# Performance work log

Hardware: AMD Instinct MI355X
Metric: run time of the kernel (lower is better)

## Reference

```python
import jax, jax.numpy as jnp
import numpy as np

B, N, T, D, H = 4, 8, 512, 256, 8
DK = D // H


def _dwconv(x, w, b=None):
    # x: (BN, D, T) depthwise conv, kernel 3, padding 'same', groups=D
    y = jax.lax.conv_general_dilated(
        x, w, window_strides=(1,), padding='SAME',
        feature_group_count=x.shape[1],
        dimension_numbers=('NCH', 'OIH', 'NCH'))
    if b is not None:
        y = y + b[None, :, None]
    return y


def setup_inputs() -> dict:
    key = jax.random.key(0)
    ks = jax.random.split(key, 16)
    s = 1.0 / np.sqrt(D)
    s3 = 1.0 / np.sqrt(3 * D)
    inp = {
        'query': jax.random.normal(ks[0], (B, N, T, D), jnp.float32),
        'key': jax.random.normal(ks[1], (B, N, T, D), jnp.float32),
        'value': jax.random.normal(ks[2], (B, N, T, D), jnp.float32),
        'key_padding_mask': jax.random.randint(ks[3], (B, N, T), 0, 2, jnp.int32),
        # depthwise conv params
        'w_pos': jax.random.uniform(ks[4], (D, 1, 3), jnp.float32, -0.577, 0.577),
        'b_pos': jax.random.uniform(ks[5], (D,), jnp.float32, -0.577, 0.577),
        # physics-initialized differential operators (still learnable floats)
        'w_vel': jnp.tile(jnp.array([-1.0, 0.0, 1.0], jnp.float32)[None, None, :], (D, 1, 1)),
        'w_acc': jnp.tile(jnp.array([1.0, -2.0, 1.0], jnp.float32)[None, None, :], (D, 1, 1)),
        # fusion / projection linears (stored as (in, out))
        'Wq': jax.random.uniform(ks[6], (3 * D, D), jnp.float32, -s3, s3),
        'bq': jax.random.uniform(ks[7], (D,), jnp.float32, -s3, s3),
        'Wk': jax.random.uniform(ks[8], (3 * D, D), jnp.float32, -s3, s3),
        'bk': jax.random.uniform(ks[9], (D,), jnp.float32, -s3, s3),
        'Wv': jax.random.uniform(ks[10], (D, D), jnp.float32, -s, s),
        'bv': jax.random.uniform(ks[11], (D,), jnp.float32, -s, s),
        'Wo': jax.random.uniform(ks[12], (D, D), jnp.float32, -s, s),
        'bo': jax.random.uniform(ks[13], (D,), jnp.float32, -s, s),
    }
    return inp


def reference(query, key, value, key_padding_mask,
              w_pos, b_pos, w_vel, w_acc,
              Wq, bq, Wk, bk, Wv, bv, Wo, bo):
    b, n, t, d = query.shape
    scale = jnp.float32(1.0 / np.sqrt(DK))

    def kin_feats(x):
        xin = x.reshape(b * n, t, d).transpose(0, 2, 1)  # (BN, D, T)
        p = _dwconv(xin, w_pos, b_pos)
        v = _dwconv(xin, w_vel)
        a = _dwconv(xin, w_acc)
        return jnp.concatenate([p, v, a], axis=1).transpose(0, 2, 1)  # (BN, T, 3D)

    qc = kin_feats(query)
    kc = kin_feats(key)

    Q = (qc @ Wq + bq).reshape(b, n, t, H, DK).transpose(0, 1, 3, 2, 4)  # (B,N,H,Tq,dk)
    K = (kc @ Wk + bk).reshape(b, n, t, H, DK).transpose(0, 1, 3, 2, 4)
    V = (value @ Wv + bv).reshape(b, n, t, H, DK).transpose(0, 1, 3, 2, 4)

    scores = jnp.einsum('bnhqd,bnhkd->bnhqk', Q, K) * scale
    mask = key_padding_mask.astype(bool)[:, :, None, None, :]  # (B,N,1,1,Tk)
    scores = jnp.where(mask, jnp.float32(-1e9), scores)
    attn = jax.nn.softmax(scores, axis=-1)  # dropout is identity in eval

    ctx = jnp.einsum('bnhqk,bnhkd->bnhqd', attn, V)
    ctx = ctx.transpose(0, 1, 3, 2, 4).reshape(b, n, t, d)
    return ctx @ Wo + bo
```

## Files before the change

kernel.cpp:

```cpp
#include <hip/hip_runtime.h>
#include <math.h>


typedef __attribute__((ext_vector_type(8))) short bf16x8;
typedef __attribute__((ext_vector_type(4))) float f32x4;
typedef __attribute__((ext_vector_type(16))) float f32x16;
typedef __attribute__((ext_vector_type(4))) int i32x4;

__device__ __forceinline__ unsigned short f2bf(float f) {
    unsigned u = __float_as_uint(f);
    return (unsigned short)((u + 0x7fff + ((u >> 16) & 1)) >> 16);
}
__device__ __forceinline__ float bf2f(unsigned short h) {
    return __uint_as_float(((unsigned)h) << 16);
}
__device__ __forceinline__ float ex2(float x) {
    float r; asm("v_exp_f32 %0, %1" : "=v"(r) : "v"(x)); return r;
}
__device__ __forceinline__ int cvtpk(float lo, float hi) {
    int r; asm("v_cvt_pk_bf16_f32 %0, %1, %2" : "=v"(r) : "v"(lo), "v"(hi)); return r;
}
__device__ __forceinline__ void gll16(const void* gsrc, const void* ldst) {
    __builtin_amdgcn_global_load_lds(
        (const __attribute__((address_space(1))) unsigned int*)gsrc,
        (__attribute__((address_space(3))) unsigned int*)ldst, 16, 0, 0);
}

#define SCL (0.17677669529663689f * 1.4426950408889634f)

#define OFF_BTQ  25231360u
#define OFF_BTK  25624576u
#define OFF_BEFF 26017792u
#define OFF_WVT  26019840u
#define OFF_WOT  26150912u
#define OFF_QB   26413056u
#define OFF_KB   34801664u
#define OFF_VV   43190272u
#define OFF_CTX  51578880u

__global__ __launch_bounds__(256) void prep(const float* __restrict__ Wq,
                                            const float* __restrict__ Wk,
                                            const float* __restrict__ bq,
                                            const float* __restrict__ bk,
                                            const float* __restrict__ wp,
                                            const float* __restrict__ wv,
                                            const float* __restrict__ wa,
                                            const float* __restrict__ b_pos,
                                            const float* __restrict__ Wv,
                                            const float* __restrict__ Wo,
                                            unsigned short* __restrict__ BtQ,
                                            unsigned short* __restrict__ BtK,
                                            float* __restrict__ beff,
                                            unsigned short* __restrict__ WVT,
                                            unsigned short* __restrict__ WOT) {
    int bid = blockIdx.x;
    if (bid < 1536) {
        int idx = bid * 256 + threadIdx.x;
        int which = idx / 196608;
        int r = idx - which * 196608;
        int j = r >> 16;
        int rem = r & 65535;
        int n = rem >> 8;
        int d = rem & 255;
        const float* W = which ? Wk : Wq;
        float val = wp[d * 3 + j] * W[d * 256 + n]
                  + wv[d * 3 + j] * W[(256 + d) * 256 + n]
                  + wa[d * 3 + j] * W[(512 + d) * 256 + n];
        if (!which) val *= SCL;
        (which ? BtK : BtQ)[n * 768 + j * 256 + d] = f2bf(val);
    } else if (bid < 2048) {
        int idx = (bid - 1536) * 256 + threadIdx.x;
        int which = idx >> 16;
        int r = idx & 65535;
        int n = r >> 8, k = r & 255;
        if (!which) {
            WVT[n * 256 + k] = f2bf(Wv[k * 256 + n]);
        } else {
            float v = Wo[k * 256 + n];
            unsigned short hi = f2bf(v);
            WOT[n * 512 + k] = hi;
            WOT[n * 512 + 256 + k] = f2bf(v - bf2f(hi));
        }
    } else {
        int which = bid - 2048;
        int n = threadIdx.x;
        const float* W = which ? Wk : Wq;
        const float* bb = which ? bk : bq;
        float s = bb[n];
        for (int d = 0; d < 256; ++d) s = fmaf(b_pos[d], W[d * 256 + n], s);
        if (!which) s *= SCL;
        beff[which * 256 + n] = s;
    }
}

template<int MODE, int KTOT, typename OutT>
__device__ __forceinline__ void gemm32_body(
    const void* Asrc, const unsigned short* __restrict__ Bt,
    const float* __restrict__ bias, OutT* __restrict__ Out,
    unsigned short* As, unsigned short* Bs)
{
    const int tid = threadIdx.x;
    const int wid = tid >> 6, l = tid & 63;
    const int l31 = l & 31, h2 = l >> 5;
    const int m0 = blockIdx.x * 64;
    const int arow = tid >> 2, aq = tid & 3;

    f32x16 acc[2][2] = {};
    f32x4 ar[4];

    auto issueB = [&](int k0, int b) {
        #pragma unroll
        for (int rr = 0; rr < 8; ++rr) {
            int row = rr * 32 + (tid >> 3);
            int srcc = ((tid & 7) ^ (row & 7)) * 8;
            gll16(Bt + (size_t)row * KTOT + k0 + srcc,
                  Bs + b * 16384 + (rr * 256 + wid * 64) * 8);
        }
    };
    auto issueA = [&](int k0, int b) {
        if constexpr (MODE == 0) {
            const unsigned short* A = (const unsigned short*)Asrc;
            #pragma unroll
            for (int rr = 0; rr < 2; ++rr) {
                int row = rr * 32 + (tid >> 3);
                int srcc = ((tid & 7) ^ (row & 7)) * 8;
                gll16(A + (size_t)(m0 + row) * 256 + (k0 & 255) + srcc,
                      As + b * 4096 + (rr * 256 + wid * 64) * 8);
            }
        } else {
            const float* X = (const float*)Asrc;
            bool valid = true;
            size_t off;
            if constexpr (MODE == 1) {
                int seq = m0 >> 9, t0 = m0 & 511;
                int st = t0 + arow + (k0 >> 8) - 1;
                valid = (st >= 0) && (st < 512);
                off = (size_t)(seq * 512 + st) * 256 + (k0 & 255) + aq * 16;
            } else {
                off = (size_t)(m0 + arow) * 256 + k0 + aq * 16;
            }
            #pragma unroll
            for (int i = 0; i < 4; ++i)
                ar[i] = valid ? *(const f32x4*)(X + off + i * 4) : (f32x4){0.f, 0.f, 0.f, 0.f};
        }
    };
    auto commitA = [&](int b) {
        if constexpr (MODE != 0) {
            i32x4 w0 = {cvtpk(ar[0][0], ar[0][1]), cvtpk(ar[0][2], ar[0][3]),
                        cvtpk(ar[1][0], ar[1][1]), cvtpk(ar[1][2], ar[1][3])};
            i32x4 w1 = {cvtpk(ar[2][0], ar[2][1]), cvtpk(ar[2][2], ar[2][3]),
                        cvtpk(ar[3][0], ar[3][1]), cvtpk(ar[3][2], ar[3][3])};
            int c0 = ((aq * 2) ^ (arow & 7)) * 8;
            int c1 = ((aq * 2 + 1) ^ (arow & 7)) * 8;
            *(i32x4*)&As[b * 4096 + arow * 64 + c0] = w0;
            *(i32x4*)&As[b * 4096 + arow * 64 + c1] = w1;
        }
    };

    issueA(0, 0);
    issueB(0, 0);
    commitA(0);
    __syncthreads();

    int b = 0;
    for (int k0 = 0; k0 < KTOT; k0 += 64, b ^= 1) {
        const bool more = (k0 + 64) < KTOT;
        if (more) { issueA(k0 + 64, b ^ 1); issueB(k0 + 64, b ^ 1); }
        const unsigned short* as = As + b * 4096;
        const unsigned short* bs = Bs + b * 16384;
        #pragma unroll
        for (int ks = 0; ks < 4; ++ks) {
            bf16x8 af[2], bfr[2];
            #pragma unroll
            for (int mt = 0; mt < 2; ++mt) {
                int r = mt * 32 + l31;
                af[mt] = *(const bf16x8*)&as[r * 64 + (((ks * 2 + h2) ^ (r & 7)) * 8)];
            }
            #pragma unroll
            for (int nt = 0; nt < 2; ++nt) {
                int r = wid * 64 + nt * 32 + l31;
                bfr[nt] = *(const bf16x8*)&bs[r * 64 + (((ks * 2 + h2) ^ (r & 7)) * 8)];
            }
            #pragma unroll
            for (int mt = 0; mt < 2; ++mt)
                #pragma unroll
                for (int nt = 0; nt < 2; ++nt)
                    acc[mt][nt] = __builtin_amdgcn_mfma_f32_32x32x16_bf16(af[mt], bfr[nt], acc[mt][nt], 0, 0, 0);
        }
        if (more) commitA(b ^ 1);
        __syncthreads();
    }

    #pragma unroll
    for (int nt = 0; nt < 2; ++nt) {
        const int col = wid * 64 + nt * 32 + l31;
        const float bb = bias[col];
        #pragma unroll
        for (int mt = 0; mt < 2; ++mt) {
            #pragma unroll
            for (int r = 0; r < 16; ++r) {
                const int row = m0 + mt * 32 + 4 * h2 + (r & 3) + 8 * (r >> 2);
                float v = acc[mt][nt][r] + bb;
                if constexpr (sizeof(OutT) == 2) Out[(size_t)row * 256 + col] = (OutT)f2bf(v);
                else Out[(size_t)row * 256 + col] = v;
            }
        }
    }
}

__global__ __launch_bounds__(256) void proj_fused(
    const float* __restrict__ query, const float* __restrict__ key,
    const float* __restrict__ value,
    const unsigned short* __restrict__ BTQ, const unsigned short* __restrict__ BTK,
    const unsigned short* __restrict__ WVT,
    const float* __restrict__ BEFF, const float* __restrict__ bv,
    unsigned short* __restrict__ QB, unsigned short* __restrict__ KB,
    unsigned short* __restrict__ VV)
{
    __shared__ alignas(16) unsigned short As[2 * 4096];
    __shared__ alignas(16) unsigned short Bs[2 * 16384];
    const int z = blockIdx.z;
    if (z == 0)      gemm32_body<1, 768, unsigned short>(query, BTQ, BEFF, QB, As, Bs);
    else if (z == 1) gemm32_body<1, 768, unsigned short>(key, BTK, BEFF + 256, KB, As, Bs);
    else             gemm32_body<2, 256, unsigned short>(value, WVT, bv, VV, As, Bs);
}

__global__ __launch_bounds__(256) void outproj(
    const unsigned short* __restrict__ CTX, const unsigned short* __restrict__ WOT,
    const float* __restrict__ bo, float* __restrict__ Out)
{
    __shared__ alignas(16) unsigned short As[2 * 4096];
    __shared__ alignas(16) unsigned short Bs[2 * 16384];
    gemm32_body<0, 512, float>(CTX, WOT, bo, Out, As, Bs);
}

__global__ __launch_bounds__(256) void attn_mfma(const unsigned short* __restrict__ Qb,
                                                 const unsigned short* __restrict__ Kb,
                                                 const unsigned short* __restrict__ Vv,
                                                 const int* __restrict__ mask,
                                                 unsigned short* __restrict__ ctx) {
    __shared__ alignas(16) unsigned short Qs[64 * 32];
    __shared__ alignas(16) unsigned short Ks[2][128 * 32];
    __shared__ alignas(16) unsigned short VsT[2][32 * 136];
    __shared__ float Mb[2][128];

    const int qt = blockIdx.x, bnh = blockIdx.y;
    const int bn = bnh >> 3, h = bnh & 7;
    const int tid = threadIdx.x, wid = tid >> 6, l = tid & 63;
    const int g = l >> 4, r15 = l & 15;
    const unsigned short* Qg = Qb + (size_t)bn * 512 * 256 + h * 32;
    const unsigned short* Kg = Kb + (size_t)bn * 512 * 256 + h * 32;
    const unsigned short* Vg = Vv + (size_t)bn * 512 * 256 + h * 32;
    const int* mp = mask + bn * 512;

    auto stageK = [&](int k0, int b) {
        #pragma unroll
        for (int qq = 0; qq < 2; ++qq) {
            int cidx = qq * 256 + wid * 64 + l;
            int row = cidx >> 2, csrc = ((cidx & 3) ^ (row & 3)) * 8;
            gll16(Kg + ((size_t)(k0 + row)) * 256 + csrc, &Ks[b][qq * 2048 + wid * 512]);
        }
    };

    {
        int cidx = wid * 64 + l;
        gll16(Qg + ((size_t)(qt * 64 + (cidx >> 2))) * 256 + (cidx & 3) * 8, Qs + wid * 512);
    }
    stageK(0, 0);
    {
        #pragma unroll
        for (int qq = 0; qq < 2; ++qq) {
            int key = l + 64 * qq;
            i32x4 vr = *(const i32x4*)(const void*)(Vg + (size_t)key * 256 + wid * 8);
            #pragma unroll
            for (int i = 0; i < 4; ++i) {
                unsigned u = (unsigned)vr[i];
                VsT[0][(wid * 8 + 2 * i) * 136 + key] = (unsigned short)(u & 0xffff);
                VsT[0][(wid * 8 + 2 * i + 1) * 136 + key] = (unsigned short)(u >> 16);
            }
        }
        if (tid < 128) Mb[0][tid] = (mp[tid] != 0) ? -1e9f : 0.f;
    }
    __syncthreads();

    const bf16x8 bq = *(const bf16x8*)&Qs[(wid * 16 + r15) * 32 + g * 8];

    float mrun = -1e30f, lrun = 0.f;
    f32x4 accO[2] = {};

    for (int kt = 0; kt < 4; ++kt) {
        const int cur = kt & 1, nxt = cur ^ 1;
        const int k0n = kt * 128 + 128;

        i32x4 vr[2];
        int mraw = 0;
        if (kt < 3) {
            stageK(k0n, nxt);
            #pragma unroll
            for (int qq = 0; qq < 2; ++qq)
                vr[qq] = *(const i32x4*)(const void*)(Vg + ((size_t)(k0n + l + 64 * qq)) * 256 + wid * 8);
            if (tid < 128) mraw = mp[k0n + tid];
        }

        float p[8][4];
        float rmax = -3e38f;
        __builtin_amdgcn_s_setprio(1);
        #pragma unroll
        for (int t2 = 0; t2 < 8; ++t2) {
            const int base = 32 * (t2 >> 1) + 4 * (t2 & 1);
            const int arow = base + 8 * (r15 >> 2) + (r15 & 3);
            bf16x8 ak = *(const bf16x8*)&Ks[cur][arow * 32 + ((g ^ (arow & 3)) * 8)];
            f32x4 cin = *(const f32x4*)&Mb[cur][base + 8 * g];
            f32x4 st = __builtin_amdgcn_mfma_f32_16x16x32_bf16(ak, bq, cin, 0, 0, 0);
            #pragma unroll
            for (int r = 0; r < 4; ++r) p[t2][r] = st[r];
            rmax = fmaxf(rmax, fmaxf(fmaxf(st[0], st[1]), fmaxf(st[2], st[3])));
        }
        __builtin_amdgcn_s_setprio(0);
        rmax = fmaxf(rmax, __shfl_xor(rmax, 16, 64));
        rmax = fmaxf(rmax, __shfl_xor(rmax, 32, 64));

        if (__ballot(rmax > mrun)) {
            float mnew = fmaxf(mrun, rmax);
            float fs = ex2(mrun - mnew);
            lrun *= fs;
            accO[0] *= fs;
            accO[1] *= fs;
            mrun = mnew;
        }
        float psum = 0.f;
        #pragma unroll
        for (int t2 = 0; t2 < 8; ++t2)
            #pragma unroll
            for (int r = 0; r < 4; ++r) {
                float e = ex2(p[t2][r] - mrun);
                p[t2][r] = e;
                psum += e;
            }
        psum += __shfl_xor(psum, 16, 64);
        psum += __shfl_xor(psum, 32, 64);
        lrun += psum;

        bf16x8 pb[4];
        #pragma unroll
        for (int s = 0; s < 4; ++s) {
            i32x4 bi = {cvtpk(p[2 * s][0], p[2 * s][1]), cvtpk(p[2 * s][2], p[2 * s][3]),
                        cvtpk(p[2 * s + 1][0], p[2 * s + 1][1]), cvtpk(p[2 * s + 1][2], p[2 * s + 1][3])};
            pb[s] = __builtin_bit_cast(bf16x8, bi);
        }

        __builtin_amdgcn_s_setprio(1);
        #pragma unroll
        for (int mt = 0; mt < 2; ++mt)
            #pragma unroll
            for (int s = 0; s < 4; ++s) {
                bf16x8 av = *(const bf16x8*)&VsT[cur][(mt * 16 + r15) * 136 + 32 * s + 8 * g];
                accO[mt] = __builtin_amdgcn_mfma_f32_16x16x32_bf16(av, pb[s], accO[mt], 0, 0, 0);
            }
        __builtin_amdgcn_s_setprio(0);

        if (kt < 3) {
            #pragma unroll
            for (int qq = 0; qq < 2; ++qq) {
                int key = l + 64 * qq;
                #pragma unroll
                for (int i = 0; i < 4; ++i) {
                    unsigned u = (unsigned)vr[qq][i];
                    VsT[nxt][(wid * 8 + 2 * i) * 136 + key] = (unsigned short)(u & 0xffff);
                    VsT[nxt][(wid * 8 + 2 * i + 1) * 136 + key] = (unsigned short)(u >> 16);
                }
            }
            if (tid < 128) Mb[nxt][tid] = (mraw != 0) ? -1e9f : 0.f;
        }
        __syncthreads();
    }

    const float inv = 1.f / lrun;
    const size_t orow = (size_t)bn * 512 + qt * 64 + wid * 16 + r15;
    #pragma unroll
    for (int mt = 0; mt < 2; ++mt) {
        ushort4 o;
        o.x = f2bf(accO[mt][0] * inv);
        o.y = f2bf(accO[mt][1] * inv);
        o.z = f2bf(accO[mt][2] * inv);
        o.w = f2bf(accO[mt][3] * inv);
        *(ushort4*)&ctx[orow * 256 + h * 32 + mt * 16 + 4 * g] = o;
    }
}

extern "C" void kernel_launch(void* const* d_in, const int* in_sizes, int n_in,
                              void* d_out, int out_size, void* d_ws, size_t ws_size,
                              hipStream_t stream) {
    const float* query = (const float*)d_in[0];
    const float* key   = (const float*)d_in[1];
    const float* value = (const float*)d_in[2];
    const int*   kpm   = (const int*)d_in[3];
    const float* w_pos = (const float*)d_in[4];
    const float* b_pos = (const float*)d_in[5];
    const float* w_vel = (const float*)d_in[6];
    const float* w_acc = (const float*)d_in[7];
    const float* Wq    = (const float*)d_in[8];
    const float* bq    = (const float*)d_in[9];
    const float* Wk    = (const float*)d_in[10];
    const float* bk    = (const float*)d_in[11];
    const float* Wv    = (const float*)d_in[12];
    const float* bv    = (const float*)d_in[13];
    const float* Wo    = (const float*)d_in[14];
    const float* bo    = (const float*)d_in[15];

    unsigned char* w = (unsigned char*)d_ws;
    unsigned short* BTQ = (unsigned short*)(w + OFF_BTQ);
    unsigned short* BTK = (unsigned short*)(w + OFF_BTK);
    float*          BEFF= (float*)(w + OFF_BEFF);
    unsigned short* WVT = (unsigned short*)(w + OFF_WVT);
    unsigned short* WOT = (unsigned short*)(w + OFF_WOT);
    unsigned short* QB  = (unsigned short*)(w + OFF_QB);
    unsigned short* KB  = (unsigned short*)(w + OFF_KB);
    unsigned short* VV  = (unsigned short*)(w + OFF_VV);
    unsigned short* CTX = (unsigned short*)(w + OFF_CTX);

    prep<<<2050, 256, 0, stream>>>(Wq, Wk, bq, bk, w_pos, w_vel, w_acc, b_pos,
                                   Wv, Wo, BTQ, BTK, BEFF, WVT, WOT);

    proj_fused<<<dim3(256, 1, 3), 256, 0, stream>>>(query, key, value, BTQ, BTK, WVT,
                                                    BEFF, bv, QB, KB, VV);

    attn_mfma<<<dim3(8, 256), 256, 0, stream>>>(QB, KB, VV, kpm, CTX);

    outproj<<<256, 256, 0, stream>>>(CTX, WOT, bo, (float*)d_out);
}
```

Measured before the change: 95.17 us.

## Retile projection GEMMs to 128x128 blocks with a 2x2 wave layout and single-buffered LDS

Changes the shared GEMM body from 64-row x 256-column block tiles to 128x128 tiles, each wave computing a 64x64 quadrant. The launch grids become 2D (128x2 blocks) so the N dimension is split across blocks. The LDS double buffering is replaced by a single buffer with two barriers per k-step, while the fp32 A register prefetch stays. This cuts shared memory per block from about 80KB to 32KB to raise occupancy and balance A/B reuse, at the cost of less overlap between loads and MFMA inside one block.

```diff
diff --git a/kernel.cpp b/kernel.cpp
--- a/kernel.cpp
+++ b/kernel.cpp
@@ -102,84 +102,80 @@
     const int tid = threadIdx.x;
     const int wid = tid >> 6, l = tid & 63;
     const int l31 = l & 31, h2 = l >> 5;
-    const int m0 = blockIdx.x * 64;
-    const int arow = tid >> 2, aq = tid & 3;
+    const int wm = wid >> 1, wn = wid & 1;
+    const int m0 = blockIdx.x * 128, n0 = blockIdx.y * 128;
+    const int arow = tid >> 1, acb = (tid & 1) * 32;
 
     f32x16 acc[2][2] = {};
-    f32x4 ar[4];
-
-    auto issueB = [&](int k0, int b) {
-        #pragma unroll
-        for (int rr = 0; rr < 8; ++rr) {
-            int row = rr * 32 + (tid >> 3);
-            int srcc = ((tid & 7) ^ (row & 7)) * 8;
-            gll16(Bt + (size_t)row * KTOT + k0 + srcc,
-                  Bs + b * 16384 + (rr * 256 + wid * 64) * 8);
+    f32x4 ar[8];
+
+    auto issueB = [&](int k0) {
+        #pragma unroll
+        for (int q = 0; q < 4; ++q) {
+            int cidx = q * 256 + wid * 64 + l;
+            int row = cidx >> 3, c = cidx & 7;
+            gll16(Bt + (size_t)(n0 + row) * KTOT + k0 + ((c ^ (row & 7)) * 8),
+                  Bs + (q * 256 + wid * 64) * 8);
         }
     };
-    auto issueA = [&](int k0, int b) {
-        if constexpr (MODE == 0) {
-            const unsigned short* A = (const unsigned short*)Asrc;
-            #pragma unroll
-            for (int rr = 0; rr < 2; ++rr) {
-                int row = rr * 32 + (tid >> 3);
-                int srcc = ((tid & 7) ^ (row & 7)) * 8;
-                gll16(A + (size_t)(m0 + row) * 256 + (k0 & 255) + srcc,
-                      As + b * 4096 + (rr * 256 + wid * 64) * 8);
-            }
+    auto issueA_lds = [&](int k0) {
+        const unsigned short* A = (const unsigned short*)Asrc;
+        #pragma unroll
+        for (int q = 0; q < 4; ++q) {
+            int cidx = q * 256 + wid * 64 + l;
+            int row = cidx >> 3, c = cidx & 7;
+            gll16(A + (size_t)(m0 + row) * 256 + (k0 & 255) + ((c ^ (row & 7)) * 8),
+                  As + (q * 256 + wid * 64) * 8);
+        }
+    };
+    auto issueA_reg = [&](int k0) {
+        const float* X = (const float*)Asrc;
+        bool valid = true;
+        size_t off;
+        if constexpr (MODE == 1) {
+            int seq = m0 >> 9, t0 = m0 & 511;
+            int st = t0 + arow + (k0 >> 8) - 1;
+            valid = (st >= 0) && (st < 512);
+            off = (size_t)(seq * 512 + (valid ? st : 0)) * 256 + (k0 & 255) + acb;
         } else {
-            const float* X = (const float*)Asrc;
-            bool valid = true;
-            size_t off;
-            if constexpr (MODE == 1) {
-                int seq = m0 >> 9, t0 = m0 & 511;
-                int st = t0 + arow + (k0 >> 8) - 1;
-                valid = (st >= 0) && (st < 512);
-                off = (size_t)(seq * 512 + st) * 256 + (k0 & 255) + aq * 16;
-            } else {
-                off = (size_t)(m0 + arow) * 256 + k0 + aq * 16;
-            }
-            #pragma unroll
-            for (int i = 0; i < 4; ++i)
-                ar[i] = valid ? *(const f32x4*)(X + off + i * 4) : (f32x4){0.f, 0.f, 0.f, 0.f};
-        }
+            off = (size_t)(m0 + arow) * 256 + k0 + acb;
+        }
+        #pragma unroll
+        for (int i = 0; i < 8; ++i)
+            ar[i] = valid ? *(const f32x4*)(X + off + i * 4) : (f32x4){0.f, 0.f, 0.f, 0.f};
     };
-    auto commitA = [&](int b) {
+    auto commitA = [&]() {
+        #pragma unroll
+        for (int i = 0; i < 4; ++i) {
+            i32x4 wv = {cvtpk(ar[2 * i][0], ar[2 * i][1]), cvtpk(ar[2 * i][2], ar[2 * i][3]),
+                        cvtpk(ar[2 * i + 1][0], ar[2 * i + 1][1]), cvtpk(ar[2 * i + 1][2], ar[2 * i + 1][3])};
+            int c = ((acb >> 3) + i) ^ (arow & 7);
+            *(i32x4*)&As[arow * 64 + c * 8] = wv;
+        }
+    };
+
+    if constexpr (MODE != 0) issueA_reg(0);
+
+    for (int k0 = 0; k0 < KTOT; k0 += 64) {
+        __syncthreads();
+        if constexpr (MODE != 0) commitA(); else issueA_lds(k0);
+        issueB(k0);
+        __syncthreads();
         if constexpr (MODE != 0) {
-            i32x4 w0 = {cvtpk(ar[0][0], ar[0][1]), cvtpk(ar[0][2], ar[0][3]),
-                        cvtpk(ar[1][0], ar[1][1]), cvtpk(ar[1][2], ar[1][3])};
-            i32x4 w1 = {cvtpk(ar[2][0], ar[2][1]), cvtpk(ar[2][2], ar[2][3]),
-                        cvtpk(ar[3][0], ar[3][1]), cvtpk(ar[3][2], ar[3][3])};
-            int c0 = ((aq * 2) ^ (arow & 7)) * 8;
-            int c1 = ((aq * 2 + 1) ^ (arow & 7)) * 8;
-            *(i32x4*)&As[b * 4096 + arow * 64 + c0] = w0;
-            *(i32x4*)&As[b * 4096 + arow * 64 + c1] = w1;
-        }
-    };
-
-    issueA(0, 0);
-    issueB(0, 0);
-    commitA(0);
-    __syncthreads();
-
-    int b = 0;
-    for (int k0 = 0; k0 < KTOT; k0 += 64, b ^= 1) {
-        const bool more = (k0 + 64) < KTOT;
-        if (more) { issueA(k0 + 64, b ^ 1); issueB(k0 + 64, b ^ 1); }
-        const unsigned short* as = As + b * 4096;
-        const unsigned short* bs = Bs + b * 16384;
+            if (k0 + 64 < KTOT) issueA_reg(k0 + 64);
+        }
         #pragma unroll
         for (int ks = 0; ks < 4; ++ks) {
             bf16x8 af[2], bfr[2];
             #pragma unroll
             for (int mt = 0; mt < 2; ++mt) {
-                int r = mt * 32 + l31;
-                af[mt] = *(const bf16x8*)&as[r * 64 + (((ks * 2 + h2) ^ (r & 7)) * 8)];
+                int r = wm * 64 + mt * 32 + l31;
+                af[mt] = *(const bf16x8*)&As[r * 64 + (((ks * 2 + h2) ^ (r & 7)) * 8)];
             }
             #pragma unroll
             for (int nt = 0; nt < 2; ++nt) {
-                int r = wid * 64 + nt * 32 + l31;
-                bfr[nt] = *(const bf16x8*)&bs[r * 64 + (((ks * 2 + h2) ^ (r & 7)) * 8)];
+                int r = wn * 64 + nt * 32 + l31;
+                bfr[nt] = *(const bf16x8*)&Bs[r * 64 + (((ks * 2 + h2) ^ (r & 7)) * 8)];
             }
             #pragma unroll
             for (int mt = 0; mt < 2; ++mt)
@@ -187,19 +183,17 @@
                 for (int nt = 0; nt < 2; ++nt)
                     acc[mt][nt] = __builtin_amdgcn_mfma_f32_32x32x16_bf16(af[mt], bfr[nt], acc[mt][nt], 0, 0, 0);
         }
-        if (more) commitA(b ^ 1);
-        __syncthreads();
     }
 
     #pragma unroll
     for (int nt = 0; nt < 2; ++nt) {
-        const int col = wid * 64 + nt * 32 + l31;
+        const int col = n0 + wn * 64 + nt * 32 + l31;
         const float bb = bias[col];
         #pragma unroll
         for (int mt = 0; mt < 2; ++mt) {
             #pragma unroll
             for (int r = 0; r < 16; ++r) {
-                const int row = m0 + mt * 32 + 4 * h2 + (r & 3) + 8 * (r >> 2);
+                const int row = m0 + wm * 64 + mt * 32 + 4 * h2 + (r & 3) + 8 * (r >> 2);
                 float v = acc[mt][nt][r] + bb;
                 if constexpr (sizeof(OutT) == 2) Out[(size_t)row * 256 + col] = (OutT)f2bf(v);
                 else Out[(size_t)row * 256 + col] = v;
@@ -217,8 +211,8 @@
     unsigned short* __restrict__ QB, unsigned short* __restrict__ KB,
     unsigned short* __restrict__ VV)
 {
-    __shared__ alignas(16) unsigned short As[2 * 4096];
-    __shared__ alignas(16) unsigned short Bs[2 * 16384];
+    __shared__ alignas(16) unsigned short As[8192];
+    __shared__ alignas(16) unsigned short Bs[8192];
     const int z = blockIdx.z;
     if (z == 0)      gemm32_body<1, 768, unsigned short>(query, BTQ, BEFF, QB, As, Bs);
     else if (z == 1) gemm32_body<1, 768, unsigned short>(key, BTK, BEFF + 256, KB, As, Bs);
@@ -229,8 +223,8 @@
     const unsigned short* __restrict__ CTX, const unsigned short* __restrict__ WOT,
     const float* __restrict__ bo, float* __restrict__ Out)
 {
-    __shared__ alignas(16) unsigned short As[2 * 4096];
-    __shared__ alignas(16) unsigned short Bs[2 * 16384];
+    __shared__ alignas(16) unsigned short As[8192];
+    __shared__ alignas(16) unsigned short Bs[8192];
     gemm32_body<0, 512, float>(CTX, WOT, bo, Out, As, Bs);
 }
 
@@ -422,10 +416,10 @@
     prep<<<2050, 256, 0, stream>>>(Wq, Wk, bq, bk, w_pos, w_vel, w_acc, b_pos,
                                    Wv, Wo, BTQ, BTK, BEFF, WVT, WOT);
 
-    proj_fused<<<dim3(256, 1, 3), 256, 0, stream>>>(query, key, value, BTQ, BTK, WVT,
+    proj_fused<<<dim3(128, 2, 3), 256, 0, stream>>>(query, key, value, BTQ, BTK, WVT,
                                                     BEFF, bv, QB, KB, VV);
 
     attn_mfma<<<dim3(8, 256), 256, 0, stream>>>(QB, KB, VV, kpm, CTX);
 
-    outproj<<<256, 256, 0, stream>>>(CTX, WOT, bo, (float*)d_out);
-}
+    outproj<<<dim3(128, 2), 256, 0, stream>>>(CTX, WOT, bo, (float*)d_out);
+}
```

New measurement: 103.7 us. 1.09x slower.
